# Kernel optimization log

Measured on AMD Instinct MI355X. Metric: run time of the kernel, lower is better.

Reference implementation:

```python
import jax, jax.numpy as jnp
import numpy as np
from jax import lax

B, V, C, D, H, W = 1, 5, 32, 48, 128, 160
RATIO = 8


def setup_inputs() -> dict:
    key = jax.random.key(0)
    k1, k2, k3 = jax.random.split(key, 3)
    features = jax.random.normal(k1, (V, B, C, H, W), jnp.float32)
    # proj_matrices[b, v, 0] = 4x4 extrinsic, proj_matrices[b, v, 1, :3, :3] = intrinsic K
    f = 200.0
    K = np.array([[f, 0.0, W / 2.0], [0.0, f, H / 2.0], [0.0, 0.0, 1.0]], np.float32)
    proj = np.zeros((B, V, 2, 4, 4), np.float32)
    for v in range(V):
        E = np.eye(4, dtype=np.float32)
        E[0, 3] = 2.0 * v  # horizontal baseline per source view
        proj[:, v, 0] = E
        P1 = np.eye(4, dtype=np.float32)
        P1[:3, :3] = K
        proj[:, v, 1] = P1
    proj_matrices = jnp.asarray(proj)
    depth_values = jnp.broadcast_to(jnp.linspace(425.0, 935.0, D, dtype=jnp.float32), (B, D))
    mask = jax.random.normal(k2, (B, 9 * RATIO * RATIO, H, W), jnp.float32)
    W_reg = jax.random.normal(k3, (1, C, 3, 3, 3), jnp.float32) * 0.05
    return {"features": features, "proj_matrices": proj_matrices,
            "depth_values": depth_values, "mask": mask, "W_reg": W_reg}


def _combine(p):
    # p: [B,2,4,4] -> K @ E[:3,:4] written into top 3 rows of extrinsic (as in source)
    top = jnp.einsum('bij,bjk->bik', p[:, 1, :3, :3], p[:, 0, :3, :4])
    return p[:, 0].at[:, :3, :4].set(top)


def _bilinear_sample(src, x, y):
    # src [B,C,H,W]; x,y [B,P] pixel coords; zeros padding, align_corners=True
    Bs, Cs, Hs, Ws = src.shape
    x0 = jnp.floor(x)
    y0 = jnp.floor(y)
    wx = x - x0
    wy = y - y0
    src_flat = src.reshape(Bs, Cs, Hs * Ws)

    def gather(xi, yi, w):
        valid = (xi >= 0) & (xi <= Ws - 1) & (yi >= 0) & (yi <= Hs - 1)
        xi_c = jnp.clip(xi, 0, Ws - 1).astype(jnp.int32)
        yi_c = jnp.clip(yi, 0, Hs - 1).astype(jnp.int32)
        idx = (yi_c * Ws + xi_c)[:, None, :]
        vals = jnp.take_along_axis(src_flat, jnp.broadcast_to(idx, (Bs, Cs, idx.shape[-1])), axis=2)
        return vals * (w * valid)[:, None, :]

    return (gather(x0, y0, (1 - wx) * (1 - wy)) + gather(x0 + 1, y0, wx * (1 - wy))
            + gather(x0, y0 + 1, (1 - wx) * wy) + gather(x0 + 1, y0 + 1, wx * wy))


def _homo_warp(src_fea, src_proj, ref_proj, depth_values):
    # faithful homo_warping2: project ref pixel grid at each depth hypothesis into src view
    Bs, Cs, Hs, Ws = src_fea.shape
    Dd = depth_values.shape[1]
    proj = jnp.einsum('bij,bjk->bik', src_proj, jnp.linalg.inv(ref_proj))
    rot = proj[:, :3, :3]
    trans = proj[:, :3, 3]
    ys, xs = jnp.meshgrid(jnp.arange(Hs, dtype=src_fea.dtype), jnp.arange(Ws, dtype=src_fea.dtype), indexing='ij')
    xyz = jnp.stack([xs.ravel(), ys.ravel(), jnp.ones(Hs * Ws, dtype=src_fea.dtype)])  # [3,HW]
    rot_xyz = jnp.einsum('bij,jp->bip', rot, xyz)  # [B,3,HW]
    pts = rot_xyz[:, :, None, :] * depth_values[:, None, :, None] + trans[:, :, None, None]  # [B,3,D,HW]
    gx = pts[:, 0] / pts[:, 2]
    gy = pts[:, 1] / pts[:, 2]
    warped = _bilinear_sample(src_fea, gx.reshape(Bs, -1), gy.reshape(Bs, -1))
    return warped.reshape(Bs, Cs, Dd, Hs, Ws)


def _convex_upsample(depth, mask, r):
    # depth [N,1,H,W], mask [N,9*r*r,H,W] -> [N, r*H, r*W]
    N, _, Hh, Ww = depth.shape
    m = jax.nn.softmax(mask.reshape(N, 1, 9, r, r, Hh, Ww), axis=2)
    dp = jnp.pad(depth, ((0, 0), (0, 0), (1, 1), (1, 1)))
    nb = jnp.stack([dp[:, :, dy:dy + Hh, dx:dx + Ww] for dy in range(3) for dx in range(3)], axis=2)
    up = jnp.sum(m * nb[:, :, :, None, None], axis=2)  # [N,1,r,r,H,W]
    up = up.transpose(0, 1, 4, 2, 5, 3)  # [N,1,H,r,W,r]
    return up.reshape(N, r * Hh, r * Ww)


def reference(features, proj_matrices, depth_values, mask, W_reg):
    num_views = features.shape[0]
    Dd = depth_values.shape[1]
    ref_proj = _combine(proj_matrices[:, 0])
    # variance cost-volume accumulation over views (ref volume broadcast along D)
    vsum = features[0][:, :, None, :, :]
    vsq = vsum ** 2
    for v in range(1, num_views):
        src_proj = _combine(proj_matrices[:, v])
        wv = _homo_warp(features[v], src_proj, ref_proj, depth_values)
        vsum = vsum + wv
        vsq = vsq + wv * wv
    variance = vsq / num_views - (vsum / num_views) ** 2  # [B,C,D,H,W]
    # cost regularization stand-in: 3x3x3 conv C->1, SAME padding
    pre = lax.conv_general_dilated(variance, W_reg, (1, 1, 1), 'SAME',
                                   dimension_numbers=('NCDHW', 'OIDHW', 'NCDHW'))[:, 0]
    prob = jax.nn.softmax(pre, axis=1)  # [B,D,H,W]
    depth = jnp.sum(prob * depth_values[:, :, None, None], axis=1)  # [B,H,W]
    # photometric confidence (no-grad path): sliding sum of 4 along D, pad (1,2)
    pd = jnp.pad(prob, ((0, 0), (1, 2), (0, 0), (0, 0)))
    sum4 = pd[:, 0:Dd] + pd[:, 1:Dd + 1] + pd[:, 2:Dd + 2] + pd[:, 3:Dd + 3]
    di = jnp.sum(prob * jnp.arange(Dd, dtype=prob.dtype)[None, :, None, None], axis=1).astype(jnp.int32)
    di = jnp.clip(di, 0, Dd - 1)
    conf = jax.lax.stop_gradient(jnp.take_along_axis(sum4, di[:, None], axis=1)[:, 0])
    depth_up = _convex_upsample(depth[:, None], mask, RATIO)
    return (depth_up, depth, conf)
```

## Files before the change

### kernel.cpp

```cpp
#include <hip/hip_runtime.h>
#include <hip/hip_bf16.h>


#define NV 5
#define NC 32
#define ND 48
#define NH 128
#define NW 160
#define HW (NH * NW)
#define DHW (ND * HW)

typedef __attribute__((ext_vector_type(2))) float f32x2;

#define OFF_M      0
#define OFF_WF     256
#define OFF_DEPTHF 4096
#define OFF_PRE    86016
#define OFF_WV     4018176

__global__ void k_setup(const float* __restrict__ proj,
                        const float* __restrict__ wreg,
                        float* __restrict__ M, float* __restrict__ wf) {
  if (threadIdx.x != 0) return;
  double P[NV][2][4][4];
  for (int v = 0; v < NV; ++v)
    for (int m = 0; m < 2; ++m)
      for (int i = 0; i < 4; ++i)
        for (int j = 0; j < 4; ++j)
          P[v][m][i][j] = (double)proj[((v * 2 + m) * 4 + i) * 4 + j];
  double C[NV][4][4];
  for (int v = 0; v < NV; ++v) {
    for (int i = 0; i < 4; ++i)
      for (int j = 0; j < 4; ++j) C[v][i][j] = P[v][0][i][j];
    for (int i = 0; i < 3; ++i)
      for (int j = 0; j < 4; ++j) {
        double s = 0.0;
        for (int k = 0; k < 3; ++k) s += P[v][1][i][k] * P[v][0][k][j];
        C[v][i][j] = s;
      }
  }
  double a[4][8];
  for (int i = 0; i < 4; ++i)
    for (int j = 0; j < 4; ++j) { a[i][j] = C[0][i][j]; a[i][j + 4] = (i == j) ? 1.0 : 0.0; }
  for (int col = 0; col < 4; ++col) {
    int piv = col; double best = fabs(a[col][col]);
    for (int r = col + 1; r < 4; ++r) { double v = fabs(a[r][col]); if (v > best) { best = v; piv = r; } }
    if (piv != col)
      for (int j = 0; j < 8; ++j) { double t = a[col][j]; a[col][j] = a[piv][j]; a[piv][j] = t; }
    double pv = a[col][col];
    for (int j = 0; j < 8; ++j) a[col][j] /= pv;
    for (int r = 0; r < 4; ++r) if (r != col) {
      double f = a[r][col];
      for (int j = 0; j < 8; ++j) a[r][j] -= f * a[col][j];
    }
  }
  double inv[4][4];
  for (int i = 0; i < 4; ++i)
    for (int j = 0; j < 4; ++j) inv[i][j] = a[i][j + 4];
  for (int v = 1; v < NV; ++v) {
    float* m = M + (v - 1) * 12;
    for (int i = 0; i < 3; ++i) {
      double r[4] = {0, 0, 0, 0};
      for (int k = 0; k < 4; ++k) {
        double cv = C[v][i][k];
        for (int j = 0; j < 4; ++j) r[j] += cv * inv[k][j];
      }
      m[i * 3 + 0] = (float)r[0]; m[i * 3 + 1] = (float)r[1]; m[i * 3 + 2] = (float)r[2];
      m[9 + i] = (float)r[3];
    }
  }
  for (int c = 0; c < NC; ++c) {
    for (int t = 0; t < 27; ++t) wf[c * 28 + t] = wreg[c * 27 + t];
    wf[c * 28 + 27] = 0.f;
  }
}

__global__ __launch_bounds__(256) void k_warpvar(
    const float* __restrict__ feat,
    const float* __restrict__ depthv,
    const float* __restrict__ M,
    const float* __restrict__ wf,
    __hip_bfloat16* __restrict__ WV)
{
  int idx = blockIdx.x * 256 + threadIdx.x;
  int x = idx % NW;
  int t1 = idx / NW;
  int y = t1 % NH;
  int d = t1 / NH;
  float xf = (float)x, yf = (float)y;
  float df = depthv[d];

  int   cidx[16];
  float cw[16];
#pragma unroll
  for (int v = 0; v < 4; ++v) {
    const float* m = M + v * 12;
    float rx = m[0] * xf + m[1] * yf + m[2];
    float ry = m[3] * xf + m[4] * yf + m[5];
    float rz = m[6] * xf + m[7] * yf + m[8];
    float px = rx * df + m[9];
    float py = ry * df + m[10];
    float pz = rz * df + m[11];
    float gx = px / pz;
    float gy = py / pz;
    float x0 = floorf(gx), y0 = floorf(gy);
    float wx = gx - x0, wy = gy - y0;
    float cxs[2] = {x0, x0 + 1.f}, cys[2] = {y0, y0 + 1.f};
    float wxs[2] = {1.f - wx, wx}, wys[2] = {1.f - wy, wy};
#pragma unroll
    for (int cy = 0; cy < 2; ++cy)
#pragma unroll
      for (int cx = 0; cx < 2; ++cx) {
        float fx = cxs[cx], fy = cys[cy];
        bool valid = (fx >= 0.f) && (fx <= (float)(NW - 1)) &&
                     (fy >= 0.f) && (fy <= (float)(NH - 1));
        float fxc = fminf(fmaxf(fx, 0.f), (float)(NW - 1));
        float fyc = fminf(fmaxf(fy, 0.f), (float)(NH - 1));
        int xi = (int)fxc, yi = (int)fyc;
        cidx[v * 4 + cy * 2 + cx] = yi * NW + xi;
        cw[v * 4 + cy * 2 + cx] = wxs[cx] * wys[cy] * (valid ? 1.f : 0.f);
      }
  }

  int pix = y * NW + x;
  f32x2 wv[14];
#pragma unroll
  for (int u = 0; u < 14; ++u) wv[u] = (f32x2){0.f, 0.f};

#pragma unroll
  for (int c = 0; c < NC; ++c) {
    float f0 = feat[c * HW + pix];
    float vs = f0, vq = f0 * f0;
#pragma unroll
    for (int v = 0; v < 4; ++v) {
      const float* fv = feat + ((v + 1) * NC + c) * HW;
      float val = cw[v * 4 + 0] * fv[cidx[v * 4 + 0]]
                + cw[v * 4 + 1] * fv[cidx[v * 4 + 1]]
                + cw[v * 4 + 2] * fv[cidx[v * 4 + 2]]
                + cw[v * 4 + 3] * fv[cidx[v * 4 + 3]];
      vs += val;
      vq += val * val;
    }
    float var = vq * 0.2f - (vs * 0.2f) * (vs * 0.2f);
    const f32x2* wrow = (const f32x2*)(wf + c * 28);
    f32x2 vv; vv.x = var; vv.y = var;
#pragma unroll
    for (int u = 0; u < 14; ++u) wv[u] += wrow[u] * vv;
  }

#pragma unroll
  for (int u = 0; u < 14; ++u) {
    int t0 = 2 * u;
    WV[t0 * DHW + idx] = __float2bfloat16(wv[u].x);
    if (t0 + 1 < 27) WV[(t0 + 1) * DHW + idx] = __float2bfloat16(wv[u].y);
  }
}

__global__ __launch_bounds__(256) void k_conv(const __hip_bfloat16* __restrict__ WV,
                                              float* __restrict__ pre) {
  int idx = blockIdx.x * 256 + threadIdx.x;
  int x = idx % NW;
  int t1 = idx / NW;
  int y = t1 % NH;
  int d = t1 / NH;
  float acc = 0.f;
#pragma unroll
  for (int dd = 0; dd < 3; ++dd) {
    int dp = d + dd - 1;
    bool dok = (dp >= 0) && (dp < ND);
    int dpc = min(max(dp, 0), ND - 1);
#pragma unroll
    for (int i = 0; i < 3; ++i) {
      int yp = y + i - 1;
      bool yok = (yp >= 0) && (yp < NH);
      int ypc = min(max(yp, 0), NH - 1);
#pragma unroll
      for (int j = 0; j < 3; ++j) {
        int xp = x + j - 1;
        bool xok = (xp >= 0) && (xp < NW);
        int xpc = min(max(xp, 0), NW - 1);
        int t = dd * 9 + i * 3 + j;
        float v = __bfloat162float(WV[t * DHW + dpc * HW + ypc * NW + xpc]);
        acc += (dok && yok && xok) ? v : 0.f;
      }
    }
  }
  pre[idx] = acc;
}

__global__ __launch_bounds__(256) void k_softmax(const float* __restrict__ pre,
                                                 const float* __restrict__ depthv,
                                                 float* __restrict__ depthf,
                                                 float* __restrict__ out_depth,
                                                 float* __restrict__ out_conf) {
  int p = blockIdx.x * 256 + threadIdx.x;
  float pr[ND];
  float m = -1e30f;
#pragma unroll
  for (int d = 0; d < ND; ++d) { pr[d] = pre[d * HW + p]; m = fmaxf(m, pr[d]); }
  float s = 0.f;
#pragma unroll
  for (int d = 0; d < ND; ++d) { pr[d] = expf(pr[d] - m); s += pr[d]; }
  float inv = 1.f / s;
  float dep = 0.f, ti = 0.f;
#pragma unroll
  for (int d = 0; d < ND; ++d) {
    float prob = pr[d] * inv;
    pr[d] = prob;
    dep += prob * depthv[d];
    ti += prob * (float)d;
  }
  int di = (int)ti;
  di = di < 0 ? 0 : (di > ND - 1 ? ND - 1 : di);
  float conf = 0.f;
#pragma unroll
  for (int d = 0; d < ND; ++d)
    conf += (d >= di - 1 && d <= di + 2) ? pr[d] : 0.f;
  depthf[p] = dep;
  out_depth[p] = dep;
  out_conf[p] = conf;
}

__global__ __launch_bounds__(256) void k_upsample(const float* __restrict__ mask,
                                                  const float* __restrict__ depthf,
                                                  float* __restrict__ out) {
  int idx = blockIdx.x * 256 + threadIdx.x;
  int fx = idx % (NW * 8);
  int fy = idx / (NW * 8);
  int x = fx >> 3, dx = fx & 7;
  int y = fy >> 3, dy = fy & 7;
  float mv[9];
  float mmax = -1e30f;
#pragma unroll
  for (int k = 0; k < 9; ++k) {
    mv[k] = mask[((k * 8 + dy) * 8 + dx) * HW + y * NW + x];
    mmax = fmaxf(mmax, mv[k]);
  }
  float s = 0.f;
#pragma unroll
  for (int k = 0; k < 9; ++k) { mv[k] = expf(mv[k] - mmax); s += mv[k]; }
  float acc = 0.f;
#pragma unroll
  for (int k = 0; k < 9; ++k) {
    int ky = y + k / 3 - 1;
    int kx = x + k % 3 - 1;
    bool ok = (ky >= 0) && (ky < NH) && (kx >= 0) && (kx < NW);
    int kyc = min(max(ky, 0), NH - 1);
    int kxc = min(max(kx, 0), NW - 1);
    float dv = depthf[kyc * NW + kxc];
    acc += mv[k] * (ok ? dv : 0.f);
  }
  out[idx] = acc / s;
}

extern "C" void kernel_launch(void* const* d_in, const int* in_sizes, int n_in,
                              void* d_out, int out_size, void* d_ws, size_t ws_size,
                              hipStream_t stream) {
  const float* feat   = (const float*)d_in[0];
  const float* proj   = (const float*)d_in[1];
  const float* depthv = (const float*)d_in[2];
  const float* mask   = (const float*)d_in[3];
  const float* wreg   = (const float*)d_in[4];

  char* ws = (char*)d_ws;
  float* M       = (float*)(ws + OFF_M);
  float* wf      = (float*)(ws + OFF_WF);
  float* depthf  = (float*)(ws + OFF_DEPTHF);
  float* pre     = (float*)(ws + OFF_PRE);
  __hip_bfloat16* WV = (__hip_bfloat16*)(ws + OFF_WV);

  float* out = (float*)d_out;
  float* out_depth = out + (NH * 8) * (NW * 8);
  float* out_conf  = out_depth + HW;

  k_setup<<<1, 64, 0, stream>>>(proj, wreg, M, wf);
  k_warpvar<<<DHW / 256, 256, 0, stream>>>(feat, depthv, M, wf, WV);
  k_conv<<<DHW / 256, 256, 0, stream>>>(WV, pre);
  k_softmax<<<HW / 256, 256, 0, stream>>>(pre, depthv, depthf, out_depth, out_conf);
  k_upsample<<<(NH * 8 * NW * 8) / 256, 256, 0, stream>>>(mask, depthf, out);
}
```

Measured before the change: 275.7 us.

## Transpose features to channel-last, fold x-taps into warp kernel, coalesce upsample

```diff
diff --git a/kernel.cpp b/kernel.cpp
--- a/kernel.cpp
+++ b/kernel.cpp
@@ -11,12 +11,14 @@
 #define DHW (ND * HW)
 
 typedef __attribute__((ext_vector_type(2))) float f32x2;
+typedef __attribute__((ext_vector_type(4))) float f32x4;
 
 #define OFF_M      0
 #define OFF_WF     256
 #define OFF_DEPTHF 4096
 #define OFF_PRE    86016
-#define OFF_WV     4018176
+#define OFF_FEATT  4018176
+#define OFF_U      17125376
 
 __global__ void k_setup(const float* __restrict__ proj,
                         const float* __restrict__ wreg,
@@ -75,22 +77,41 @@
   }
 }
 
-__global__ __launch_bounds__(256) void k_warpvar(
-    const float* __restrict__ feat,
+__global__ __launch_bounds__(256) void k_transpose(const float* __restrict__ feat,
+                                                   float* __restrict__ featT) {
+  int v = blockIdx.x / 80;
+  int pix0 = (blockIdx.x % 80) * 256;
+  int pix = pix0 + threadIdx.x;
+  float r[NC];
+#pragma unroll
+  for (int c = 0; c < NC; ++c)
+    r[c] = feat[((size_t)(v * NC + c)) * HW + pix];
+  float* dst = featT + ((size_t)v * HW + pix) * NC;
+#pragma unroll
+  for (int g = 0; g < 8; ++g) {
+    f32x4 val; val.x = r[4*g]; val.y = r[4*g+1]; val.z = r[4*g+2]; val.w = r[4*g+3];
+    *(f32x4*)(dst + 4 * g) = val;
+  }
+}
+
+__global__ __launch_bounds__(320) void k_warpvar(
+    const float* __restrict__ featT,
     const float* __restrict__ depthv,
     const float* __restrict__ M,
     const float* __restrict__ wf,
-    __hip_bfloat16* __restrict__ WV)
+    __hip_bfloat16* __restrict__ U)
 {
-  int idx = blockIdx.x * 256 + threadIdx.x;
-  int x = idx % NW;
-  int t1 = idx / NW;
-  int y = t1 % NH;
-  int d = t1 / NH;
+  __shared__ float lds[27 * 320];
+  int tid = threadIdx.x;
+  int d = blockIdx.x / 64;
+  int rem = (blockIdx.x % 64) * 320 + tid;
+  int y = rem / NW;
+  int x = rem % NW;
+  int idx = d * HW + rem;
   float xf = (float)x, yf = (float)y;
   float df = depthv[d];
 
-  int   cidx[16];
+  const float* cp[16];
   float cw[16];
 #pragma unroll
   for (int v = 0; v < 4; ++v) {
@@ -117,46 +138,63 @@
         float fxc = fminf(fmaxf(fx, 0.f), (float)(NW - 1));
         float fyc = fminf(fmaxf(fy, 0.f), (float)(NH - 1));
         int xi = (int)fxc, yi = (int)fyc;
-        cidx[v * 4 + cy * 2 + cx] = yi * NW + xi;
+        cp[v * 4 + cy * 2 + cx] = featT + ((size_t)(v + 1) * HW + yi * NW + xi) * NC;
         cw[v * 4 + cy * 2 + cx] = wxs[cx] * wys[cy] * (valid ? 1.f : 0.f);
       }
   }
-
-  int pix = y * NW + x;
-  f32x2 wv[14];
-#pragma unroll
-  for (int u = 0; u < 14; ++u) wv[u] = (f32x2){0.f, 0.f};
-
-#pragma unroll
-  for (int c = 0; c < NC; ++c) {
-    float f0 = feat[c * HW + pix];
-    float vs = f0, vq = f0 * f0;
+  const float* rp = featT + (size_t)rem * NC;
+
+  f32x2 wv2[14];
+#pragma unroll
+  for (int u = 0; u < 14; ++u) wv2[u] = (f32x2){0.f, 0.f};
+
+#pragma unroll
+  for (int g = 0; g < 8; ++g) {
+    f32x4 rv = *(const f32x4*)(rp + 4 * g);
+    f32x4 vs = rv;
+    f32x4 vq = rv * rv;
 #pragma unroll
     for (int v = 0; v < 4; ++v) {
-      const float* fv = feat + ((v + 1) * NC + c) * HW;
-      float val = cw[v * 4 + 0] * fv[cidx[v * 4 + 0]]
-                + cw[v * 4 + 1] * fv[cidx[v * 4 + 1]]
-                + cw[v * 4 + 2] * fv[cidx[v * 4 + 2]]
-                + cw[v * 4 + 3] * fv[cidx[v * 4 + 3]];
+      f32x4 l0 = *(const f32x4*)(cp[4 * v + 0] + 4 * g);
+      f32x4 l1 = *(const f32x4*)(cp[4 * v + 1] + 4 * g);
+      f32x4 l2 = *(const f32x4*)(cp[4 * v + 2] + 4 * g);
+      f32x4 l3 = *(const f32x4*)(cp[4 * v + 3] + 4 * g);
+      f32x4 val = l0 * cw[4 * v + 0] + l1 * cw[4 * v + 1]
+                + l2 * cw[4 * v + 2] + l3 * cw[4 * v + 3];
       vs += val;
       vq += val * val;
     }
-    float var = vq * 0.2f - (vs * 0.2f) * (vs * 0.2f);
-    const f32x2* wrow = (const f32x2*)(wf + c * 28);
-    f32x2 vv; vv.x = var; vv.y = var;
-#pragma unroll
-    for (int u = 0; u < 14; ++u) wv[u] += wrow[u] * vv;
-  }
-
-#pragma unroll
-  for (int u = 0; u < 14; ++u) {
-    int t0 = 2 * u;
-    WV[t0 * DHW + idx] = __float2bfloat16(wv[u].x);
-    if (t0 + 1 < 27) WV[(t0 + 1) * DHW + idx] = __float2bfloat16(wv[u].y);
-  }
-}
-
-__global__ __launch_bounds__(256) void k_conv(const __hip_bfloat16* __restrict__ WV,
+    f32x4 vsn = vs * 0.2f;
+    f32x4 var = vq * 0.2f - vsn * vsn;
+#pragma unroll
+    for (int cc = 0; cc < 4; ++cc) {
+      const f32x2* wr = (const f32x2*)(wf + (4 * g + cc) * 28);
+      float vv = var[cc];
+      f32x2 vb; vb.x = vv; vb.y = vv;
+#pragma unroll
+      for (int u = 0; u < 14; ++u) wv2[u] += wr[u] * vb;
+    }
+  }
+
+#pragma unroll
+  for (int t = 0; t < 27; ++t)
+    lds[t * 320 + tid] = (t & 1) ? wv2[t >> 1].y : wv2[t >> 1].x;
+  __syncthreads();
+
+  bool xm = (x > 0), xp = (x < NW - 1);
+  int tl = xm ? tid - 1 : tid;
+  int tr = xp ? tid + 1 : tid;
+#pragma unroll
+  for (int t9 = 0; t9 < 9; ++t9) {
+    float s = lds[(t9 * 3 + 1) * 320 + tid];
+    float sl = lds[(t9 * 3 + 0) * 320 + tl];
+    float sr = lds[(t9 * 3 + 2) * 320 + tr];
+    s += (xm ? sl : 0.f) + (xp ? sr : 0.f);
+    U[(size_t)t9 * DHW + idx] = __float2bfloat16(s);
+  }
+}
+
+__global__ __launch_bounds__(256) void k_conv(const __hip_bfloat16* __restrict__ U,
                                               float* __restrict__ pre) {
   int idx = blockIdx.x * 256 + threadIdx.x;
   int x = idx % NW;
@@ -174,15 +212,9 @@
       int yp = y + i - 1;
       bool yok = (yp >= 0) && (yp < NH);
       int ypc = min(max(yp, 0), NH - 1);
-#pragma unroll
-      for (int j = 0; j < 3; ++j) {
-        int xp = x + j - 1;
-        bool xok = (xp >= 0) && (xp < NW);
-        int xpc = min(max(xp, 0), NW - 1);
-        int t = dd * 9 + i * 3 + j;
-        float v = __bfloat162float(WV[t * DHW + dpc * HW + ypc * NW + xpc]);
-        acc += (dok && yok && xok) ? v : 0.f;
-      }
+      int t9 = dd * 3 + i;
+      float v = __bfloat162float(U[(size_t)t9 * DHW + dpc * HW + ypc * NW + x]);
+      acc += (dok && yok) ? v : 0.f;
     }
   }
   pre[idx] = acc;
@@ -221,36 +253,47 @@
   out_conf[p] = conf;
 }
 
-__global__ __launch_bounds__(256) void k_upsample(const float* __restrict__ mask,
+__global__ __launch_bounds__(640) void k_upsample(const float* __restrict__ mask,
                                                   const float* __restrict__ depthf,
                                                   float* __restrict__ out) {
-  int idx = blockIdx.x * 256 + threadIdx.x;
-  int fx = idx % (NW * 8);
-  int fy = idx / (NW * 8);
-  int x = fx >> 3, dx = fx & 7;
-  int y = fy >> 3, dy = fy & 7;
-  float mv[9];
-  float mmax = -1e30f;
-#pragma unroll
-  for (int k = 0; k < 9; ++k) {
-    mv[k] = mask[((k * 8 + dy) * 8 + dx) * HW + y * NW + x];
-    mmax = fmaxf(mmax, mv[k]);
-  }
-  float s = 0.f;
-#pragma unroll
-  for (int k = 0; k < 9; ++k) { mv[k] = expf(mv[k] - mmax); s += mv[k]; }
-  float acc = 0.f;
-#pragma unroll
-  for (int k = 0; k < 9; ++k) {
-    int ky = y + k / 3 - 1;
-    int kx = x + k % 3 - 1;
-    bool ok = (ky >= 0) && (ky < NH) && (kx >= 0) && (kx < NW);
-    int kyc = min(max(ky, 0), NH - 1);
-    int kxc = min(max(kx, 0), NW - 1);
-    float dv = depthf[kyc * NW + kxc];
-    acc += mv[k] * (ok ? dv : 0.f);
-  }
-  out[idx] = acc / s;
+  __shared__ float row[NW * 8];
+  int y = blockIdx.x >> 3;
+  int dy = blockIdx.x & 7;
+#pragma unroll
+  for (int rep = 0; rep < 2; ++rep) {
+    int lin = rep * 640 + threadIdx.x;
+    int dx = lin / NW;
+    int x = lin % NW;
+    float mv[9];
+    float mmax = -1e30f;
+#pragma unroll
+    for (int k = 0; k < 9; ++k) {
+      mv[k] = mask[(size_t)(k * 64 + dy * 8 + dx) * HW + y * NW + x];
+      mmax = fmaxf(mmax, mv[k]);
+    }
+    float s = 0.f;
+#pragma unroll
+    for (int k = 0; k < 9; ++k) { mv[k] = expf(mv[k] - mmax); s += mv[k]; }
+    float acc = 0.f;
+#pragma unroll
+    for (int k = 0; k < 9; ++k) {
+      int ky = y + k / 3 - 1;
+      int kx = x + k % 3 - 1;
+      bool ok = (ky >= 0) && (ky < NH) && (kx >= 0) && (kx < NW);
+      int kyc = min(max(ky, 0), NH - 1);
+      int kxc = min(max(kx, 0), NW - 1);
+      float dv = depthf[kyc * NW + kxc];
+      acc += mv[k] * (ok ? dv : 0.f);
+    }
+    row[x * 8 + dx] = acc / s;
+  }
+  __syncthreads();
+  float* orow = out + (size_t)(y * 8 + dy) * (NW * 8);
+#pragma unroll
+  for (int rep = 0; rep < 2; ++rep) {
+    int j = rep * 640 + threadIdx.x;
+    orow[j] = row[j];
+  }
 }
 
 extern "C" void kernel_launch(void* const* d_in, const int* in_sizes, int n_in,
@@ -267,15 +310,17 @@
   float* wf      = (float*)(ws + OFF_WF);
   float* depthf  = (float*)(ws + OFF_DEPTHF);
   float* pre     = (float*)(ws + OFF_PRE);
-  __hip_bfloat16* WV = (__hip_bfloat16*)(ws + OFF_WV);
+  float* featT   = (float*)(ws + OFF_FEATT);
+  __hip_bfloat16* U = (__hip_bfloat16*)(ws + OFF_U);
 
   float* out = (float*)d_out;
   float* out_depth = out + (NH * 8) * (NW * 8);
   float* out_conf  = out_depth + HW;
 
   k_setup<<<1, 64, 0, stream>>>(proj, wreg, M, wf);
-  k_warpvar<<<DHW / 256, 256, 0, stream>>>(feat, depthv, M, wf, WV);
-  k_conv<<<DHW / 256, 256, 0, stream>>>(WV, pre);
+  k_transpose<<<NV * 80, 256, 0, stream>>>(feat, featT);
+  k_warpvar<<<DHW / 320, 320, 0, stream>>>(featT, depthv, M, wf, U);
+  k_conv<<<DHW / 256, 256, 0, stream>>>(U, pre);
   k_softmax<<<HW / 256, 256, 0, stream>>>(pre, depthv, depthf, out_depth, out_conf);
-  k_upsample<<<(NH * 8 * NW * 8) / 256, 256, 0, stream>>>(mask, depthf, out);
-}
+  k_upsample<<<NH * 8, 640, 0, stream>>>(mask, depthf, out);
+}
```

Measured after the change: 472.6 us. +71.4%, slower.
